# Optimization experiments

Hardware: AMD Instinct MI355X
Metric: run time of the kernel (lower is better)

## Reference

```python
import jax, jax.numpy as jnp
import numpy as np

DIM = 128
NUM_HEADS = 4
WH, WW = 7, 7
N = WH * WW            # 49 tokens per window
NW = 64                # number of windows (56/7)^2
BATCH = 64
B_ = BATCH * NW        # 4096


def _relative_position_index(Wh, Ww):
    coords = np.stack(np.meshgrid(np.arange(Wh), np.arange(Ww), indexing='ij'))  # [2,Wh,Ww]
    coords = coords.reshape(2, -1)
    rel = coords[:, :, None] - coords[:, None, :]          # [2, N, N]
    rel = rel.transpose(1, 2, 0).astype(np.int64)          # [N, N, 2]
    rel[:, :, 0] += Wh - 1
    rel[:, :, 1] += Ww - 1
    rel[:, :, 0] *= 2 * Ww - 1
    return rel.sum(-1)                                     # [N, N]


def setup_inputs() -> dict:
    key = jax.random.key(0)
    ks = jax.random.split(key, 8)
    x = jax.random.normal(ks[0], (B_, N, DIM), dtype=jnp.float32)
    # Swin shift-mask: additive, 0 or large negative; random floats are fine for math check
    mask = jax.random.normal(ks[1], (NW, N, N), dtype=jnp.float32)
    qkv_w = jax.random.normal(ks[2], (DIM, 3 * DIM), dtype=jnp.float32) * 0.02
    qkv_b = jax.random.normal(ks[3], (3 * DIM,), dtype=jnp.float32) * 0.02
    proj_w = jax.random.normal(ks[4], (DIM, DIM), dtype=jnp.float32) * 0.02
    proj_b = jax.random.normal(ks[5], (DIM,), dtype=jnp.float32) * 0.02
    table_size = (2 * WH - 1) * (2 * WW - 1)  # 169
    bias_table = jax.random.normal(ks[6], (table_size, NUM_HEADS), dtype=jnp.float32) * 0.02
    rel_idx = jnp.asarray(_relative_position_index(WH, WW), dtype=jnp.int32)  # [N,N]
    return {"x": x, "mask": mask, "qkv_w": qkv_w, "qkv_b": qkv_b,
            "proj_w": proj_w, "proj_b": proj_b, "bias_table": bias_table,
            "rel_idx": rel_idx}


def reference(x, mask, qkv_w, qkv_b, proj_w, proj_b, bias_table, rel_idx):
    B, Nn, C = x.shape
    H = bias_table.shape[1]
    hd = C // H
    scale = hd ** -0.5
    # qkv projection -> [3, B, H, N, hd]
    qkv = (x @ qkv_w + qkv_b).reshape(B, Nn, 3, H, hd).transpose(2, 0, 3, 1, 4)
    q, k, v = qkv[0] * scale, qkv[1], qkv[2]
    attn = jnp.einsum('bhnd,bhmd->bhnm', q, k)  # [B,H,N,N]
    # gathered relative position bias -> [H,N,N]
    bias = bias_table[rel_idx.reshape(-1)].reshape(Nn, Nn, H).transpose(2, 0, 1)
    attn = attn + bias[None]
    nW = mask.shape[0]
    attn = attn.reshape(-1, nW, H, Nn, Nn) + mask[None, :, None].astype(attn.dtype)
    attn = jax.nn.softmax(attn.reshape(-1, H, Nn, Nn), axis=-1)
    out = jnp.einsum('bhnm,bhmd->bnhd', attn, v).reshape(B, Nn, C)
    return out @ proj_w + proj_b
```

## Files before the change

kernel.cpp:

```cpp
#include <hip/hip_runtime.h>

#define NTOK 49
#define DIMC 128
#define NH   4
#define NWIN 64
#define NBLK 4096

#define WPROJ_OFF 98304
#define BMF_OFF   131072

typedef unsigned short u16x8 __attribute__((ext_vector_type(8)));
typedef __bf16        bf16x8 __attribute__((ext_vector_type(8)));
typedef float         f32x4  __attribute__((ext_vector_type(4)));

__device__ __forceinline__ unsigned short f2bf(float f) {
  return __builtin_bit_cast(unsigned short, (__bf16)f);
}

__device__ __forceinline__ bf16x8 ld_frag(const unsigned short* p) {
  return __builtin_bit_cast(bf16x8, *(const u16x8*)p);
}

__device__ __forceinline__ bf16x8 pack_bf16x8(float4 lo, float4 hi) {
  bf16x8 r;
  r[0] = (__bf16)lo.x; r[1] = (__bf16)lo.y; r[2] = (__bf16)lo.z; r[3] = (__bf16)lo.w;
  r[4] = (__bf16)hi.x; r[5] = (__bf16)hi.y; r[6] = (__bf16)hi.z; r[7] = (__bf16)hi.w;
  return r;
}

#define MFMA(a, b, c) __builtin_amdgcn_mfma_f32_16x16x32_bf16(a, b, c, 0, 0, 0)

__global__ void prep_kernel(const float* __restrict__ qkv_w,
                            const float* __restrict__ proj_w,
                            const float* __restrict__ bias_table,
                            const int*   __restrict__ rel_idx,
                            const float* __restrict__ mask,
                            unsigned short* __restrict__ wqkv,
                            unsigned short* __restrict__ wproj,
                            float* __restrict__ bmf)
{
  const int tid = blockIdx.x * blockDim.x + threadIdx.x;
  const int nth = gridDim.x * blockDim.x;

  for (int idx = tid; idx < 4*24*64*8; idx += nth) {
    int ii = idx & 7, lane = (idx >> 3) & 63, rest = idx >> 9;
    int ct = rest % 24, kt = rest / 24;
    int k = kt*32 + ((lane >> 4) << 3) + ii;
    int c = ct*16 + (lane & 15);
    wqkv[idx] = f2bf(qkv_w[k*384 + c]);
  }
  for (int idx = tid; idx < 4*8*64*8; idx += nth) {
    int ii = idx & 7, lane = (idx >> 3) & 63, rest = idx >> 9;
    int ct = rest & 7, kt = rest >> 3;
    int k = kt*32 + ((lane >> 4) << 3) + ii;
    int c = ct*16 + (lane & 15);
    wproj[idx] = f2bf(proj_w[k*128 + c]);
  }
  for (int idx = tid; idx < NWIN*NH*16*256; idx += nth) {
    int r2   = idx & 3;
    int lane = (idx >> 2) & 63;
    int ij   = (idx >> 8) & 15;
    int h    = (idx >> 12) & 3;
    int wi   = idx >> 14;
    int i = ij >> 2, j = ij & 3;
    int r = i*16 + ((lane >> 4) << 2) + r2;
    int c = j*16 + (lane & 15);
    float v = -1e30f;
    if (r < NTOK && c < NTOK)
      v = mask[wi*2401 + r*49 + c] + bias_table[rel_idx[r*49 + c]*4 + h];
    bmf[idx] = v;
  }
}

#define SLOT 5772
__global__ __launch_bounds__(256, 3) void winattn_kernel(
    const float* __restrict__ x,
    const float* __restrict__ qkv_b,
    const float* __restrict__ proj_b,
    const unsigned short* __restrict__ wqkv,
    const unsigned short* __restrict__ wproj,
    const float* __restrict__ bmf,
    float* __restrict__ out)
{
  __shared__ __align__(16) unsigned short smem[24112];

  const int b    = blockIdx.x;
  const int wi   = b & (NWIN - 1);
  const int tid  = threadIdx.x;
  const int h    = tid >> 6;
  const int lane = tid & 63;
  const int lhi  = lane >> 4;
  const int llo  = lane & 15;

  unsigned short* slot = smem + h*SLOT;
  unsigned short* Qh  = slot;
  unsigned short* Kh  = slot + 1764;
  unsigned short* Vh  = slot + 3528;
  unsigned short* Ph  = slot;
  unsigned short* XOh = slot;

  const f32x4 zv = {0.f, 0.f, 0.f, 0.f};
  const float* xb = x + (size_t)b * (NTOK*DIMC);

  f32x4 acc[6][4];
  #pragma unroll
  for (int j = 0; j < 6; j++)
    #pragma unroll
    for (int i = 0; i < 4; i++) acc[j][i] = zv;

  #pragma unroll
  for (int kt = 0; kt < 4; kt++) {
    bf16x8 a[4];
    #pragma unroll
    for (int i = 0; i < 4; i++) {
      float4 lo = make_float4(0.f,0.f,0.f,0.f), hi = lo;
      int row = i*16 + llo;
      if (i < 3 || row < NTOK) {
        const float4* p = (const float4*)(xb + row*DIMC + kt*32 + lhi*8);
        lo = p[0]; hi = p[1];
      }
      a[i] = pack_bf16x8(lo, hi);
    }
    #pragma unroll
    for (int j = 0; j < 6; j++) {
      int ct = (j >> 1)*8 + h*2 + (j & 1);
      bf16x8 bw = ld_frag(wqkv + (((kt*24 + ct)*64 + lane) << 3));
      #pragma unroll
      for (int i = 0; i < 4; i++) acc[j][i] = MFMA(a[i], bw, acc[j][i]);
    }
  }

  float bias[6];
  #pragma unroll
  for (int j = 0; j < 6; j++)
    bias[j] = qkv_b[((j >> 1)*8 + h*2 + (j & 1))*16 + llo];

  const float scale = 0.17677669529663687f;

  #pragma unroll
  for (int j = 0; j < 2; j++) {
    int d = j*16 + llo;
    #pragma unroll
    for (int i = 0; i < 4; i++)
      #pragma unroll
      for (int r2 = 0; r2 < 4; r2++) {
        int r = i*16 + lhi*4 + r2;
        if (r < NTOK) Qh[r*36 + d] = f2bf((acc[j][i][r2] + bias[j]) * scale);
      }
  }

  float4 bmv[16];
  {
    const float4* bmf4 = (const float4*)bmf + (size_t)(wi*4 + h)*16*64 + lane;
    #pragma unroll
    for (int t = 0; t < 16; t++) bmv[t] = bmf4[t*64];
  }

  #pragma unroll
  for (int j = 2; j < 4; j++) {
    int d = (j - 2)*16 + llo;
    #pragma unroll
    for (int i = 0; i < 4; i++)
      #pragma unroll
      for (int r2 = 0; r2 < 4; r2++) {
        int r = i*16 + lhi*4 + r2;
        if (r < NTOK) Kh[r*36 + d] = f2bf(acc[j][i][r2] + bias[j]);
      }
  }
  #pragma unroll
  for (int j = 4; j < 6; j++) {
    int d = (j - 4)*16 + llo;
    #pragma unroll
    for (int i = 0; i < 4; i++) {
      ushort4 pk;
      pk.x = f2bf(acc[j][i][0] + bias[j]);
      pk.y = f2bf(acc[j][i][1] + bias[j]);
      pk.z = f2bf(acc[j][i][2] + bias[j]);
      pk.w = f2bf(acc[j][i][3] + bias[j]);
      *(ushort4*)(Vh + d*68 + i*16 + lhi*4) = pk;
    }
  }
  Vh[32*68 + lane] = 0x3F80;

  f32x4 s[4][4];
  #pragma unroll
  for (int i = 0; i < 4; i++)
    #pragma unroll
    for (int j = 0; j < 4; j++) s[i][j] = zv;

  {
    bf16x8 qa[4];
    #pragma unroll
    for (int i = 0; i < 4; i++) qa[i] = ld_frag(Qh + (i*16 + llo)*36 + lhi*8);
    #pragma unroll
    for (int j = 0; j < 4; j++) {
      bf16x8 kb = ld_frag(Kh + (j*16 + llo)*36 + lhi*8);
      #pragma unroll
      for (int i = 0; i < 4; i++) s[i][j] = MFMA(qa[i], kb, s[i][j]);
    }
  }

  #pragma unroll
  for (int j = 0; j < 4; j++) {
    bool cok = (j*16 + llo) < NTOK;
    #pragma unroll
    for (int i = 0; i < 4; i++) {
      float4 t = bmv[i*4 + j];
      #pragma unroll
      for (int r2 = 0; r2 < 4; r2++) {
        float v = s[i][j][r2] + (&t.x)[r2];
        s[i][j][r2] = __expf(cok ? v : -1e30f);
      }
    }
  }

  #pragma unroll
  for (int i = 0; i < 4; i++)
    #pragma unroll
    for (int r2 = 0; r2 < 4; r2++) {
      int r = i*16 + lhi*4 + r2;
      if (r < NTOK) {
        #pragma unroll
        for (int j = 0; j < 4; j++)
          Ph[r*72 + j*16 + llo] = f2bf(s[i][j][r2]);
      }
    }

  f32x4 oacc[2][4], osum[4];
  #pragma unroll
  for (int i = 0; i < 4; i++) { oacc[0][i] = zv; oacc[1][i] = zv; osum[i] = zv; }

  #pragma unroll
  for (int ks = 0; ks < 2; ks++) {
    bf16x8 pa[4];
    #pragma unroll
    for (int i = 0; i < 4; i++)
      pa[i] = ld_frag(Ph + (i*16 + llo)*72 + ks*32 + lhi*8);
    #pragma unroll
    for (int nt = 0; nt < 3; nt++) {
      bf16x8 vb = ld_frag(Vh + (nt*16 + llo)*68 + ks*32 + lhi*8);
      #pragma unroll
      for (int i = 0; i < 4; i++) {
        if (nt < 2) oacc[nt][i] = MFMA(pa[i], vb, oacc[nt][i]);
        else        osum[i]     = MFMA(pa[i], vb, osum[i]);
      }
    }
  }

  #pragma unroll
  for (int i = 0; i < 4; i++)
    #pragma unroll
    for (int r2 = 0; r2 < 4; r2++) {
      float sm  = __shfl(osum[i][r2], lane & 48, 64);
      float inv = __builtin_amdgcn_rcpf(sm);
      oacc[0][i][r2] *= inv;
      oacc[1][i][r2] *= inv;
    }

  #pragma unroll
  for (int nt = 0; nt < 2; nt++)
    #pragma unroll
    for (int i = 0; i < 4; i++)
      #pragma unroll
      for (int r2 = 0; r2 < 4; r2++) {
        int r = i*16 + lhi*4 + r2;
        if (r < NTOK) XOh[r*36 + nt*16 + llo] = f2bf(oacc[nt][i][r2]);
      }

  __syncthreads();

  {
    f32x4 pacc[2][4];
    #pragma unroll
    for (int j = 0; j < 2; j++)
      #pragma unroll
      for (int i = 0; i < 4; i++) pacc[j][i] = zv;

    #pragma unroll
    for (int kt = 0; kt < 4; kt++) {
      bf16x8 a[4];
      #pragma unroll
      for (int i = 0; i < 4; i++)
        a[i] = ld_frag(smem + kt*SLOT + (i*16 + llo)*36 + lhi*8);
      #pragma unroll
      for (int j = 0; j < 2; j++) {
        int ct = h*2 + j;
        bf16x8 bw = ld_frag(wproj + (((kt*8 + ct)*64 + lane) << 3));
        #pragma unroll
        for (int i = 0; i < 4; i++) pacc[j][i] = MFMA(a[i], bw, pacc[j][i]);
      }
    }

    float* op = out + (size_t)b * (NTOK*DIMC);
    #pragma unroll
    for (int j = 0; j < 2; j++) {
      int c = (h*2 + j)*16 + llo;
      float pb = proj_b[c];
      #pragma unroll
      for (int i = 0; i < 4; i++)
        #pragma unroll
        for (int r2 = 0; r2 < 4; r2++) {
          int r = i*16 + lhi*4 + r2;
          if (r < NTOK) op[r*128 + c] = pacc[j][i][r2] + pb;
        }
    }
  }
}

extern "C" void kernel_launch(void* const* d_in, const int* in_sizes, int n_in,
                              void* d_out, int out_size, void* d_ws, size_t ws_size,
                              hipStream_t stream)
{
  const float* x          = (const float*)d_in[0];
  const float* mask       = (const float*)d_in[1];
  const float* qkv_w      = (const float*)d_in[2];
  const float* qkv_b      = (const float*)d_in[3];
  const float* proj_w     = (const float*)d_in[4];
  const float* proj_b     = (const float*)d_in[5];
  const float* bias_table = (const float*)d_in[6];
  const int*   rel_idx    = (const int*)d_in[7];
  float* out = (float*)d_out;

  unsigned short* wqkv  = (unsigned short*)d_ws;
  unsigned short* wproj = (unsigned short*)((char*)d_ws + WPROJ_OFF);
  float*          bmf   = (float*)((char*)d_ws + BMF_OFF);

  prep_kernel<<<1024, 256, 0, stream>>>(qkv_w, proj_w, bias_table, rel_idx, mask,
                                        wqkv, wproj, bmf);
  winattn_kernel<<<NBLK, 256, 0, stream>>>(x, qkv_b, proj_b, wqkv, wproj, bmf, out);
}
```

Before: 127.8 us.

## Split each head across two waves with 512-thread blocks

Doubles the block to 512 threads so each attention head is handled by two waves. The QKV columns, query row tiles and projection output columns are divided between the wave pair, which cuts per-wave accumulator registers and raises parallelism per window. Four block-wide barriers are added to share Q/K/V/P through LDS between the paired waves. The cost is more synchronization, and each wave of a pair still loads the full x tile for the QKV GEMM.

New measurement: 186.3 us. 1.46x slower.

```diff
diff --git a/kernel.cpp b/kernel.cpp
--- a/kernel.cpp
+++ b/kernel.cpp
@@ -73,7 +73,7 @@
 }
 
 #define SLOT 5772
-__global__ __launch_bounds__(256, 3) void winattn_kernel(
+__global__ __launch_bounds__(512, 5) void winattn_kernel(
     const float* __restrict__ x,
     const float* __restrict__ qkv_b,
     const float* __restrict__ proj_b,
@@ -87,7 +87,9 @@
   const int b    = blockIdx.x;
   const int wi   = b & (NWIN - 1);
   const int tid  = threadIdx.x;
-  const int h    = tid >> 6;
+  const int wave = tid >> 6;
+  const int h    = wave & 3;
+  const int ws   = wave >> 2;
   const int lane = tid & 63;
   const int lhi  = lane >> 4;
   const int llo  = lane & 15;
@@ -102,11 +104,11 @@
   const f32x4 zv = {0.f, 0.f, 0.f, 0.f};
   const float* xb = x + (size_t)b * (NTOK*DIMC);
 
-  f32x4 acc[6][4];
-  #pragma unroll
-  for (int j = 0; j < 6; j++)
-    #pragma unroll
-    for (int i = 0; i < 4; i++) acc[j][i] = zv;
+  f32x4 acc[3][4];
+  #pragma unroll
+  for (int jj = 0; jj < 3; jj++)
+    #pragma unroll
+    for (int i = 0; i < 4; i++) acc[jj][i] = zv;
 
   #pragma unroll
   for (int kt = 0; kt < 4; kt++) {
@@ -122,81 +124,76 @@
       a[i] = pack_bf16x8(lo, hi);
     }
     #pragma unroll
-    for (int j = 0; j < 6; j++) {
-      int ct = (j >> 1)*8 + h*2 + (j & 1);
+    for (int jj = 0; jj < 3; jj++) {
+      int ct = jj*8 + h*2 + ws;
       bf16x8 bw = ld_frag(wqkv + (((kt*24 + ct)*64 + lane) << 3));
       #pragma unroll
-      for (int i = 0; i < 4; i++) acc[j][i] = MFMA(a[i], bw, acc[j][i]);
-    }
-  }
-
-  float bias[6];
-  #pragma unroll
-  for (int j = 0; j < 6; j++)
-    bias[j] = qkv_b[((j >> 1)*8 + h*2 + (j & 1))*16 + llo];
+      for (int i = 0; i < 4; i++) acc[jj][i] = MFMA(a[i], bw, acc[jj][i]);
+    }
+  }
+
+  float bias[3];
+  #pragma unroll
+  for (int jj = 0; jj < 3; jj++)
+    bias[jj] = qkv_b[(jj*8 + h*2 + ws)*16 + llo];
 
   const float scale = 0.17677669529663687f;
-
-  #pragma unroll
-  for (int j = 0; j < 2; j++) {
-    int d = j*16 + llo;
-    #pragma unroll
-    for (int i = 0; i < 4; i++)
-      #pragma unroll
-      for (int r2 = 0; r2 < 4; r2++) {
-        int r = i*16 + lhi*4 + r2;
-        if (r < NTOK) Qh[r*36 + d] = f2bf((acc[j][i][r2] + bias[j]) * scale);
-      }
-  }
-
-  float4 bmv[16];
+  const int d = ws*16 + llo;
+
+  #pragma unroll
+  for (int i = 0; i < 4; i++)
+    #pragma unroll
+    for (int r2 = 0; r2 < 4; r2++) {
+      int r = i*16 + lhi*4 + r2;
+      if (r < NTOK) Qh[r*36 + d] = f2bf((acc[0][i][r2] + bias[0]) * scale);
+    }
+
+  float4 bmv[8];
   {
     const float4* bmf4 = (const float4*)bmf + (size_t)(wi*4 + h)*16*64 + lane;
     #pragma unroll
-    for (int t = 0; t < 16; t++) bmv[t] = bmf4[t*64];
-  }
-
-  #pragma unroll
-  for (int j = 2; j < 4; j++) {
-    int d = (j - 2)*16 + llo;
-    #pragma unroll
-    for (int i = 0; i < 4; i++)
-      #pragma unroll
-      for (int r2 = 0; r2 < 4; r2++) {
-        int r = i*16 + lhi*4 + r2;
-        if (r < NTOK) Kh[r*36 + d] = f2bf(acc[j][i][r2] + bias[j]);
-      }
-  }
-  #pragma unroll
-  for (int j = 4; j < 6; j++) {
-    int d = (j - 4)*16 + llo;
-    #pragma unroll
-    for (int i = 0; i < 4; i++) {
-      ushort4 pk;
-      pk.x = f2bf(acc[j][i][0] + bias[j]);
-      pk.y = f2bf(acc[j][i][1] + bias[j]);
-      pk.z = f2bf(acc[j][i][2] + bias[j]);
-      pk.w = f2bf(acc[j][i][3] + bias[j]);
-      *(ushort4*)(Vh + d*68 + i*16 + lhi*4) = pk;
-    }
-  }
-  Vh[32*68 + lane] = 0x3F80;
-
-  f32x4 s[4][4];
+    for (int il = 0; il < 2; il++)
+      #pragma unroll
+      for (int j = 0; j < 4; j++)
+        bmv[il*4 + j] = bmf4[((ws*2 + il)*4 + j)*64];
+  }
+
   #pragma unroll
   for (int i = 0; i < 4; i++)
     #pragma unroll
-    for (int j = 0; j < 4; j++) s[i][j] = zv;
+    for (int r2 = 0; r2 < 4; r2++) {
+      int r = i*16 + lhi*4 + r2;
+      if (r < NTOK) Kh[r*36 + d] = f2bf(acc[1][i][r2] + bias[1]);
+    }
+  #pragma unroll
+  for (int i = 0; i < 4; i++) {
+    ushort4 pk;
+    pk.x = f2bf(acc[2][i][0] + bias[2]);
+    pk.y = f2bf(acc[2][i][1] + bias[2]);
+    pk.z = f2bf(acc[2][i][2] + bias[2]);
+    pk.w = f2bf(acc[2][i][3] + bias[2]);
+    *(ushort4*)(Vh + d*68 + i*16 + lhi*4) = pk;
+  }
+  if (ws == 0) Vh[32*68 + lane] = 0x3F80;
+
+  __syncthreads();
+
+  f32x4 s[2][4];
+  #pragma unroll
+  for (int il = 0; il < 2; il++)
+    #pragma unroll
+    for (int j = 0; j < 4; j++) s[il][j] = zv;
 
   {
-    bf16x8 qa[4];
-    #pragma unroll
-    for (int i = 0; i < 4; i++) qa[i] = ld_frag(Qh + (i*16 + llo)*36 + lhi*8);
+    bf16x8 qa[2];
+    #pragma unroll
+    for (int il = 0; il < 2; il++)
+      qa[il] = ld_frag(Qh + ((ws*2 + il)*16 + llo)*36 + lhi*8);
     #pragma unroll
     for (int j = 0; j < 4; j++) {
       bf16x8 kb = ld_frag(Kh + (j*16 + llo)*36 + lhi*8);
       #pragma unroll
-      for (int i = 0; i < 4; i++) s[i][j] = MFMA(qa[i], kb, s[i][j]);
+      for (int il = 0; il < 2; il++) s[il][j] = MFMA(qa[il], kb, s[il][j]);
     }
   }
 
@@ -204,106 +201,101 @@
   for (int j = 0; j < 4; j++) {
     bool cok = (j*16 + llo) < NTOK;
     #pragma unroll
-    for (int i = 0; i < 4; i++) {
-      float4 t = bmv[i*4 + j];
+    for (int il = 0; il < 2; il++) {
+      float4 t = bmv[il*4 + j];
       #pragma unroll
       for (int r2 = 0; r2 < 4; r2++) {
-        float v = s[i][j][r2] + (&t.x)[r2];
-        s[i][j][r2] = __expf(cok ? v : -1e30f);
-      }
-    }
-  }
-
-  #pragma unroll
-  for (int i = 0; i < 4; i++)
+        float v = s[il][j][r2] + (&t.x)[r2];
+        s[il][j][r2] = __expf(cok ? v : -1e30f);
+      }
+    }
+  }
+
+  #pragma unroll
+  for (int il = 0; il < 2; il++)
     #pragma unroll
     for (int r2 = 0; r2 < 4; r2++) {
-      int r = i*16 + lhi*4 + r2;
+      int r = (ws*2 + il)*16 + lhi*4 + r2;
       if (r < NTOK) {
         #pragma unroll
         for (int j = 0; j < 4; j++)
-          Ph[r*72 + j*16 + llo] = f2bf(s[i][j][r2]);
-      }
-    }
-
-  f32x4 oacc[2][4], osum[4];
-  #pragma unroll
-  for (int i = 0; i < 4; i++) { oacc[0][i] = zv; oacc[1][i] = zv; osum[i] = zv; }
+          Ph[r*72 + j*16 + llo] = f2bf(s[il][j][r2]);
+      }
+    }
+
+  __syncthreads();
+
+  f32x4 oacc[2][2], osum[2];
+  #pragma unroll
+  for (int il = 0; il < 2; il++) { oacc[0][il] = zv; oacc[1][il] = zv; osum[il] = zv; }
 
   #pragma unroll
   for (int ks = 0; ks < 2; ks++) {
-    bf16x8 pa[4];
-    #pragma unroll
-    for (int i = 0; i < 4; i++)
-      pa[i] = ld_frag(Ph + (i*16 + llo)*72 + ks*32 + lhi*8);
+    bf16x8 pa[2];
+    #pragma unroll
+    for (int il = 0; il < 2; il++)
+      pa[il] = ld_frag(Ph + ((ws*2 + il)*16 + llo)*72 + ks*32 + lhi*8);
     #pragma unroll
     for (int nt = 0; nt < 3; nt++) {
       bf16x8 vb = ld_frag(Vh + (nt*16 + llo)*68 + ks*32 + lhi*8);
       #pragma unroll
-      for (int i = 0; i < 4; i++) {
-        if (nt < 2) oacc[nt][i] = MFMA(pa[i], vb, oacc[nt][i]);
-        else        osum[i]     = MFMA(pa[i], vb, osum[i]);
-      }
-    }
-  }
-
-  #pragma unroll
-  for (int i = 0; i < 4; i++)
+      for (int il = 0; il < 2; il++) {
+        if (nt < 2) oacc[nt][il] = MFMA(pa[il], vb, oacc[nt][il]);
+        else        osum[il]     = MFMA(pa[il], vb, osum[il]);
+      }
+    }
+  }
+
+  #pragma unroll
+  for (int il = 0; il < 2; il++)
     #pragma unroll
     for (int r2 = 0; r2 < 4; r2++) {
-      float sm  = __shfl(osum[i][r2], lane & 48, 64);
+      float sm  = __shfl(osum[il][r2], lane & 48, 64);
       float inv = __builtin_amdgcn_rcpf(sm);
-      oacc[0][i][r2] *= inv;
-      oacc[1][i][r2] *= inv;
-    }
+      oacc[0][il][r2] *= inv;
+      oacc[1][il][r2] *= inv;
+    }
+
+  __syncthreads();
 
   #pragma unroll
   for (int nt = 0; nt < 2; nt++)
+    #pragma unroll
+    for (int il = 0; il < 2; il++)
+      #pragma unroll
+      for (int r2 = 0; r2 < 4; r2++) {
+        int r = (ws*2 + il)*16 + lhi*4 + r2;
+        if (r < NTOK) XOh[r*36 + nt*16 + llo] = f2bf(oacc[nt][il][r2]);
+      }
+
+  __syncthreads();
+
+  {
+    f32x4 pacc[4];
+    #pragma unroll
+    for (int i = 0; i < 4; i++) pacc[i] = zv;
+
+    #pragma unroll
+    for (int kt = 0; kt < 4; kt++) {
+      bf16x8 a[4];
+      #pragma unroll
+      for (int i = 0; i < 4; i++)
+        a[i] = ld_frag(smem + kt*SLOT + (i*16 + llo)*36 + lhi*8);
+      bf16x8 bw = ld_frag(wproj + (((kt*8 + wave)*64 + lane) << 3));
+      #pragma unroll
+      for (int i = 0; i < 4; i++) pacc[i] = MFMA(a[i], bw, pacc[i]);
+    }
+
+    float* op = out + (size_t)b * (NTOK*DIMC);
+    int c = wave*16 + llo;
+    float pb = proj_b[c];
     #pragma unroll
     for (int i = 0; i < 4; i++)
       #pragma unroll
       for (int r2 = 0; r2 < 4; r2++) {
         int r = i*16 + lhi*4 + r2;
-        if (r < NTOK) XOh[r*36 + nt*16 + llo] = f2bf(oacc[nt][i][r2]);
-      }
-
-  __syncthreads();
-
-  {
-    f32x4 pacc[2][4];
-    #pragma unroll
-    for (int j = 0; j < 2; j++)
-      #pragma unroll
-      for (int i = 0; i < 4; i++) pacc[j][i] = zv;
-
-    #pragma unroll
-    for (int kt = 0; kt < 4; kt++) {
-      bf16x8 a[4];
-      #pragma unroll
-      for (int i = 0; i < 4; i++)
-        a[i] = ld_frag(smem + kt*SLOT + (i*16 + llo)*36 + lhi*8);
-      #pragma unroll
-      for (int j = 0; j < 2; j++) {
-        int ct = h*2 + j;
-        bf16x8 bw = ld_frag(wproj + (((kt*8 + ct)*64 + lane) << 3));
-        #pragma unroll
-        for (int i = 0; i < 4; i++) pacc[j][i] = MFMA(a[i], bw, pacc[j][i]);
-      }
-    }
-
-    float* op = out + (size_t)b * (NTOK*DIMC);
-    #pragma unroll
-    for (int j = 0; j < 2; j++) {
-      int c = (h*2 + j)*16 + llo;
-      float pb = proj_b[c];
-      #pragma unroll
-      for (int i = 0; i < 4; i++)
-        #pragma unroll
-        for (int r2 = 0; r2 < 4; r2++) {
-          int r = i*16 + lhi*4 + r2;
-          if (r < NTOK) op[r*128 + c] = pacc[j][i][r2] + pb;
-        }
-    }
+        if (r < NTOK) op[r*128 + c] = pacc[i][r2] + pb;
+      }
   }
 }
 
@@ -327,5 +319,5 @@
 
   prep_kernel<<<1024, 256, 0, stream>>>(qkv_w, proj_w, bias_table, rel_idx, mask,
                                         wqkv, wproj, bmf);
-  winattn_kernel<<<NBLK, 256, 0, stream>>>(x, qkv_b, proj_b, wqkv, wproj, bmf, out);
-}
+  winattn_kernel<<<NBLK, 512, 0, stream>>>(x, qkv_b, proj_b, wqkv, wproj, bmf, out);
+}
```

## Compute transposed attention scores to normalize softmax in registers

Applied to the files above, without the earlier changes.

Computes S^T = K·Q^T so each lane holds one query column, which lets the softmax row sum be reduced with two cross-lane shuffles instead of an extra MFMA against a ones column of V. Probabilities are normalized before storing to a swizzled shared buffer, and O^T = V^T·P^T is produced so the output is written with packed 8-byte stores. The bias/mask table is re-laid out to match the transposed fragments, the per-head shared slot grows, and MFMA sections get a raised wave priority. The larger shared footprint could reduce occupancy.

After: 113.1 us. -11.5%, faster.

```diff
diff --git a/kernel.cpp b/kernel.cpp
--- a/kernel.cpp
+++ b/kernel.cpp
@@ -62,17 +62,17 @@
     int ij   = (idx >> 8) & 15;
     int h    = (idx >> 12) & 3;
     int wi   = idx >> 14;
-    int i = ij >> 2, j = ij & 3;
-    int r = i*16 + ((lane >> 4) << 2) + r2;
-    int c = j*16 + (lane & 15);
+    int it = ij >> 2, jt = ij & 3;
+    int q = jt*16 + (lane & 15);
+    int k = it*16 + ((lane >> 4) << 2) + r2;
     float v = -1e30f;
-    if (r < NTOK && c < NTOK)
-      v = mask[wi*2401 + r*49 + c] + bias_table[rel_idx[r*49 + c]*4 + h];
+    if (q < NTOK && k < NTOK)
+      v = mask[wi*2401 + q*49 + k] + bias_table[rel_idx[q*49 + k]*4 + h];
     bmf[idx] = v;
   }
 }
 
-#define SLOT 5772
+#define SLOT 6272
 __global__ __launch_bounds__(256, 3) void winattn_kernel(
     const float* __restrict__ x,
     const float* __restrict__ qkv_b,
@@ -82,7 +82,7 @@
     const float* __restrict__ bmf,
     float* __restrict__ out)
 {
-  __shared__ __align__(16) unsigned short smem[24112];
+  __shared__ __align__(16) unsigned short smem[4*SLOT];
 
   const int b    = blockIdx.x;
   const int wi   = b & (NWIN - 1);
@@ -95,8 +95,8 @@
   unsigned short* slot = smem + h*SLOT;
   unsigned short* Qh  = slot;
   unsigned short* Kh  = slot + 1764;
-  unsigned short* Vh  = slot + 3528;
-  unsigned short* Ph  = slot;
+  unsigned short* Vh  = slot + 4096;
+  unsigned short* Pb  = slot;
   unsigned short* XOh = slot;
 
   const f32x4 zv = {0.f, 0.f, 0.f, 0.f};
@@ -145,7 +145,7 @@
       #pragma unroll
       for (int r2 = 0; r2 < 4; r2++) {
         int r = i*16 + lhi*4 + r2;
-        if (r < NTOK) Qh[r*36 + d] = f2bf((acc[j][i][r2] + bias[j]) * scale);
+        if (r < NTOK) Qh[r*36 + d] = f2bf((acc[0+j][i][r2] + bias[j]) * scale);
       }
   }
 
@@ -180,92 +180,104 @@
       *(ushort4*)(Vh + d*68 + i*16 + lhi*4) = pk;
     }
   }
-  Vh[32*68 + lane] = 0x3F80;
 
   f32x4 s[4][4];
   #pragma unroll
-  for (int i = 0; i < 4; i++)
-    #pragma unroll
-    for (int j = 0; j < 4; j++) s[i][j] = zv;
+  for (int it = 0; it < 4; it++)
+    #pragma unroll
+    for (int jt = 0; jt < 4; jt++) s[it][jt] = zv;
 
   {
-    bf16x8 qa[4];
-    #pragma unroll
-    for (int i = 0; i < 4; i++) qa[i] = ld_frag(Qh + (i*16 + llo)*36 + lhi*8);
-    #pragma unroll
-    for (int j = 0; j < 4; j++) {
-      bf16x8 kb = ld_frag(Kh + (j*16 + llo)*36 + lhi*8);
-      #pragma unroll
-      for (int i = 0; i < 4; i++) s[i][j] = MFMA(qa[i], kb, s[i][j]);
-    }
-  }
-
-  #pragma unroll
-  for (int j = 0; j < 4; j++) {
-    bool cok = (j*16 + llo) < NTOK;
-    #pragma unroll
-    for (int i = 0; i < 4; i++) {
-      float4 t = bmv[i*4 + j];
+    bf16x8 ka[4], qb[4];
+    #pragma unroll
+    for (int it = 0; it < 4; it++) ka[it] = ld_frag(Kh + (it*16 + llo)*36 + lhi*8);
+    #pragma unroll
+    for (int jt = 0; jt < 4; jt++) qb[jt] = ld_frag(Qh + (jt*16 + llo)*36 + lhi*8);
+    __builtin_amdgcn_s_setprio(1);
+    #pragma unroll
+    for (int jt = 0; jt < 4; jt++)
+      #pragma unroll
+      for (int it = 0; it < 4; it++)
+        s[it][jt] = MFMA(ka[it], qb[jt], s[it][jt]);
+    __builtin_amdgcn_s_setprio(0);
+  }
+
+  #pragma unroll
+  for (int jt = 0; jt < 4; jt++) {
+    float e[4][4];
+    float psum = 0.f;
+    #pragma unroll
+    for (int it = 0; it < 3; it++) {
+      float4 t = bmv[it*4 + jt];
       #pragma unroll
       for (int r2 = 0; r2 < 4; r2++) {
-        float v = s[i][j][r2] + (&t.x)[r2];
-        s[i][j][r2] = __expf(cok ? v : -1e30f);
-      }
-    }
-  }
-
-  #pragma unroll
-  for (int i = 0; i < 4; i++)
-    #pragma unroll
-    for (int r2 = 0; r2 < 4; r2++) {
-      int r = i*16 + lhi*4 + r2;
-      if (r < NTOK) {
-        #pragma unroll
-        for (int j = 0; j < 4; j++)
-          Ph[r*72 + j*16 + llo] = f2bf(s[i][j][r2]);
-      }
-    }
-
-  f32x4 oacc[2][4], osum[4];
-  #pragma unroll
-  for (int i = 0; i < 4; i++) { oacc[0][i] = zv; oacc[1][i] = zv; osum[i] = zv; }
+        float v = __expf(s[it][jt][r2] + (&t.x)[r2]);
+        e[it][r2] = v;
+        psum += v;
+      }
+    }
+    {
+      float v = (lhi == 0) ? __expf(s[3][jt][0] + bmv[12 + jt].x) : 0.f;
+      e[3][0] = v; e[3][1] = 0.f; e[3][2] = 0.f; e[3][3] = 0.f;
+      psum += v;
+    }
+    psum += __shfl_xor(psum, 16, 64);
+    psum += __shfl_xor(psum, 32, 64);
+    float inv = __builtin_amdgcn_rcpf(psum);
+    int q = jt*16 + llo;
+    #pragma unroll
+    for (int it = 0; it < 4; it++) {
+      ushort4 pk;
+      pk.x = f2bf(e[it][0] * inv);
+      pk.y = f2bf(e[it][1] * inv);
+      pk.z = f2bf(e[it][2] * inv);
+      pk.w = f2bf(e[it][3] * inv);
+      int el = (q*64 + it*16 + lhi*4) ^ ((llo & 7) << 3);
+      *(ushort4*)(Pb + el) = pk;
+    }
+  }
+
+  f32x4 o[2][4];
+  #pragma unroll
+  for (int mt = 0; mt < 2; mt++)
+    #pragma unroll
+    for (int nt = 0; nt < 4; nt++) o[mt][nt] = zv;
 
   #pragma unroll
   for (int ks = 0; ks < 2; ks++) {
-    bf16x8 pa[4];
-    #pragma unroll
-    for (int i = 0; i < 4; i++)
-      pa[i] = ld_frag(Ph + (i*16 + llo)*72 + ks*32 + lhi*8);
-    #pragma unroll
-    for (int nt = 0; nt < 3; nt++) {
-      bf16x8 vb = ld_frag(Vh + (nt*16 + llo)*68 + ks*32 + lhi*8);
-      #pragma unroll
-      for (int i = 0; i < 4; i++) {
-        if (nt < 2) oacc[nt][i] = MFMA(pa[i], vb, oacc[nt][i]);
-        else        osum[i]     = MFMA(pa[i], vb, osum[i]);
-      }
-    }
-  }
-
-  #pragma unroll
-  for (int i = 0; i < 4; i++)
-    #pragma unroll
-    for (int r2 = 0; r2 < 4; r2++) {
-      float sm  = __shfl(osum[i][r2], lane & 48, 64);
-      float inv = __builtin_amdgcn_rcpf(sm);
-      oacc[0][i][r2] *= inv;
-      oacc[1][i][r2] *= inv;
-    }
-
-  #pragma unroll
-  for (int nt = 0; nt < 2; nt++)
-    #pragma unroll
-    for (int i = 0; i < 4; i++)
-      #pragma unroll
-      for (int r2 = 0; r2 < 4; r2++) {
-        int r = i*16 + lhi*4 + r2;
-        if (r < NTOK) XOh[r*36 + nt*16 + llo] = f2bf(oacc[nt][i][r2]);
-      }
+    bf16x8 va[2], pbf[4];
+    #pragma unroll
+    for (int mt = 0; mt < 2; mt++)
+      va[mt] = ld_frag(Vh + (mt*16 + llo)*68 + ks*32 + lhi*8);
+    #pragma unroll
+    for (int nt = 0; nt < 4; nt++) {
+      int el = ((nt*16 + llo)*64 + ks*32 + lhi*8) ^ ((llo & 7) << 3);
+      pbf[nt] = ld_frag(Pb + el);
+    }
+    __builtin_amdgcn_s_setprio(1);
+    #pragma unroll
+    for (int nt = 0; nt < 4; nt++)
+      #pragma unroll
+      for (int mt = 0; mt < 2; mt++)
+        o[mt][nt] = MFMA(va[mt], pbf[nt], o[mt][nt]);
+    __builtin_amdgcn_s_setprio(0);
+  }
+
+  #pragma unroll
+  for (int nt = 0; nt < 4; nt++) {
+    int q = nt*16 + llo;
+    if (q < NTOK) {
+      #pragma unroll
+      for (int mt = 0; mt < 2; mt++) {
+        ushort4 pk;
+        pk.x = f2bf(o[mt][nt][0]);
+        pk.y = f2bf(o[mt][nt][1]);
+        pk.z = f2bf(o[mt][nt][2]);
+        pk.w = f2bf(o[mt][nt][3]);
+        *(ushort4*)(XOh + q*36 + mt*16 + lhi*4) = pk;
+      }
+    }
+  }
 
   __syncthreads();
 
```
